# Optimization experiments

Measured on AMD Instinct MI355X. Metric: run time of the kernel, lower is better.

Reference implementation:

```python
import jax, jax.numpy as jnp
import numpy as np

B, T, I = 32, 512, 96
H, M, R, K = 256, 6, 16, 16
TASK, SENS = 32, 64
MPG = M // 3  # mechanisms per group
OUT = 64


def setup_inputs() -> dict:
    key = jax.random.key(0)
    ks = jax.random.split(key, 12)
    inp = {
        'x': jax.random.normal(ks[0], (B, T, I), jnp.float32),
        # stacked per-mechanism LowRankRNNCell params
        'W_ip': jax.random.normal(ks[1], (M, H, H), jnp.float32) / np.sqrt(H),
        'b_ip': jnp.zeros((M, H), jnp.float32),
        'U': jax.random.normal(ks[2], (M, H, R), jnp.float32) / np.sqrt(R),
        'Vr': jax.random.normal(ks[3], (M, R, H), jnp.float32) / np.sqrt(H),
        'cell_bias': jnp.zeros((M, H), jnp.float32),
        'W_in_task': 0.01 * jax.random.normal(ks[4], (MPG, TASK, H), jnp.float32),
        'W_in_sensory': 0.01 * jax.random.normal(ks[5], (MPG, SENS, H), jnp.float32),
        'W_Q': 0.01 * jax.random.normal(ks[6], (M, H, K), jnp.float32),
        'W_K': 0.01 * jax.random.normal(ks[7], (M, H, K), jnp.float32),
        'W_V': 0.01 * jax.random.normal(ks[8], (M, H, H), jnp.float32),
        'W_out': jax.random.normal(ks[9], (H * MPG, OUT), jnp.float32) / np.sqrt(H * MPG),
        'b_out': jnp.zeros((OUT,), jnp.float32),
    }
    return inp


def _rim_forward(x, W_ip, b_ip, U, Vr, cell_bias, W_in_task, W_in_sensory,
                 W_Q, W_K, W_V, W_out, b_out):
    scale = jnp.float32(1.0 / np.sqrt(K))

    def step(Hs, x_t):
        # input routing: group 0 <- task input, group 1 <- sensory, group 2 <- zeros
        x_task = x_t[:, -TASK:]
        x_sens = x_t[:, :-TASK]
        g0 = jnp.einsum('bi,mih->bmh', x_task, W_in_task)
        g1 = jnp.einsum('bi,mih->bmh', x_sens, W_in_sensory)
        A_in = jnp.concatenate([g0, g1, jnp.zeros_like(g0)], axis=1)  # [B,M,H]
        # batched LowRankRNNCell update per mechanism
        inp_part = jnp.einsum('bmi,mih->bmh', A_in, W_ip) + b_ip
        rec = jnp.einsum('bmr,mrh->bmh', jnp.einsum('bmh,mhr->bmr', Hs, U), Vr)
        H_in = jnp.tanh(inp_part + rec + cell_bias)  # [B,M,H]
        # communication attention (exact einsum structure of the original)
        Qc = jnp.einsum('bmh,mhk->bmk', H_in, W_Q)
        Kc = jnp.einsum('bmh,mhk->bmk', H_in, W_K)
        Vc = jnp.einsum('bmh,mhj->bjm', H_in, W_V)  # V_comm[b,h,m]
        attn = jax.nn.softmax(jnp.einsum('bmk,bnk->bmn', Qc, Kc) * scale, axis=-1)
        A_comm = jnp.einsum('bmn,bhm->bnh', attn, Vc)
        H_new = H_in + A_comm
        out = H_new[:, -MPG:].reshape(H_new.shape[0], -1) @ W_out + b_out
        return H_new, (out, H_new, A_in, A_comm, attn)

    H0 = jnp.zeros((x.shape[0], M, H), x.dtype)
    _, (outs, Hseq, Ain_seq, Acomm_seq, attn_seq) = jax.lax.scan(
        step, H0, jnp.swapaxes(x, 0, 1))
    # time-major -> batch-major where the torch code stacks on dim=1 (outputs)
    outputs = jnp.swapaxes(outs, 0, 1)  # [B,T,OUT]
    return outputs, Hseq, Ain_seq, Acomm_seq, attn_seq


def reference(x, W_ip, b_ip, U, Vr, cell_bias, W_in_task, W_in_sensory,
              W_Q, W_K, W_V, W_out, b_out):
    return _rim_forward(x, W_ip, b_ip, U, Vr, cell_bias, W_in_task,
                        W_in_sensory, W_Q, W_K, W_V, W_out, b_out)
```

## Files before the change

### kernel.cpp

```cpp
#include <hip/hip_runtime.h>
#include <math.h>

#define BB 32
#define TT 512
#define II 96
#define HH 256
#define MM 6
#define OUTD 64

#define O_HSEQ  1048576
#define O_AIN   26214400
#define O_ACM   51380224
#define O_ATTN  76546048

#define WS_WEFF 0
#define WS_UT   49152
#define WS_WQT  73728
#define WS_WKT  98304
#define WS_VCH  122880
#define WS_QK   319488
#define WS_FLAG 331776
#define WS_COOP_FLOATS 332288

#define LBAR() asm volatile("s_waitcnt lgkmcnt(0)\n\ts_barrier" ::: "memory")

__global__ __launch_bounds__(256) void rim_weff(
    const float* __restrict__ Wtask, const float* __restrict__ Wsens,
    const float* __restrict__ Wip,
    const float* __restrict__ U, const float* __restrict__ WQ, const float* __restrict__ WK,
    float* __restrict__ Weff, float* __restrict__ Ut, float* __restrict__ WQt, float* __restrict__ WKt)
{
  __shared__ float row[256];
  const int bidx = blockIdx.x;
  const int tid = threadIdx.x;
  if (bidx < 192) {
    int m, i;
    if (bidx < 32)       { m = 0; i = bidx; }
    else if (bidx < 64)  { m = 1; i = bidx - 32; }
    else if (bidx < 128) { m = 2; i = bidx - 64; }
    else                 { m = 3; i = bidx - 128; }
    row[tid] = (m < 2) ? Wtask[(m * 32 + i) * 256 + tid]
                       : Wsens[((m - 2) * 64 + i) * 256 + tid];
    __syncthreads();
    float acc = 0.f;
    const float* wip = Wip + m * 65536 + tid;
    #pragma unroll 8
    for (int j = 0; j < 256; ++j) acc += row[j] * wip[j * 256];
    const int base = (m == 0) ? 0 : (m == 1) ? 8192 : (m == 2) ? 16384 : 32768;
    Weff[base + i * 256 + tid] = acc;
  } else {
    const int p = bidx - 192;
    const int m = p >> 4, r = p & 15;
    Ut [(m * 16 + r) * 256 + tid] = U [m * 4096 + tid * 16 + r];
    WQt[(m * 16 + r) * 256 + tid] = WQ[m * 4096 + tid * 16 + r];
    WKt[(m * 16 + r) * 256 + tid] = WK[m * 4096 + tid * 16 + r];
  }
}

__global__ __launch_bounds__(256) void rim_pre(
    const float* __restrict__ x,
    const float* __restrict__ Wtask, const float* __restrict__ Wsens,
    float* __restrict__ Ain)
{
  __shared__ float xr[16][96];
  const int tid = threadIdx.x;
  const int rb0 = blockIdx.x * 16;
  for (int idx = tid; idx < 16 * 96; idx += 256) {
    int r = idx / 96, c = idx % 96;
    int rb = rb0 + r; int t = rb >> 5, b = rb & 31;
    xr[r][c] = x[(b * TT + t) * II + c];
  }
  __syncthreads();
  const int h = tid;
  float acc[16];

  for (int m = 0; m < 4; ++m) {
    const int cnt  = (m < 2) ? 32 : 64;
    const int xoff = (m < 2) ? 64 : 0;
    const float* W = (m < 2) ? (Wtask + m * 32 * 256) : (Wsens + (m - 2) * 64 * 256);
    #pragma unroll
    for (int r = 0; r < 16; ++r) acc[r] = 0.f;
    for (int i = 0; i < cnt; ++i) {
      float w = W[i * 256 + h];
      #pragma unroll
      for (int r = 0; r < 16; ++r) acc[r] += xr[r][xoff + i] * w;
    }
    #pragma unroll
    for (int r = 0; r < 16; ++r) {
      int rb = rb0 + r; int t = rb >> 5, b = rb & 31;
      Ain[((t * 32 + b) * 6 + m) * 256 + h] = acc[r];
    }
  }
  #pragma unroll
  for (int r = 0; r < 16; ++r) {
    int rb = rb0 + r; int t = rb >> 5, b = rb & 31;
    Ain[((t * 32 + b) * 6 + 4) * 256 + h] = 0.f;
    Ain[((t * 32 + b) * 6 + 5) * 256 + h] = 0.f;
  }
}

__global__ __launch_bounds__(512, 2) void rim_step(
    const float* __restrict__ x,
    const float* __restrict__ Vr, const float* __restrict__ WV,
    const float* __restrict__ bip, const float* __restrict__ cbias,
    const float* __restrict__ UtW, const float* __restrict__ WQtW,
    const float* __restrict__ WKtW, const float* __restrict__ WeffW,
    float* __restrict__ VcHG, float* __restrict__ QKG,
    unsigned int* __restrict__ seqG,
    float* __restrict__ Hseq, float* __restrict__ Acm, float* __restrict__ attnO)
{
  __shared__ __align__(16) float Hl[256];
  __shared__ __align__(16) float Hin[256];
  __shared__ float biasl[256];
  __shared__ float Utl[16][257];
  __shared__ float Vrl[16][257];
  __shared__ float WQtl[16][257];
  __shared__ float WKtl[16][257];
  __shared__ float Weffl[64][256];
  __shared__ float inpl[2][256];
  __shared__ float xl[2][96];
  __shared__ float Vcp1[256];
  __shared__ float tmpUr[16];
  __shared__ float attnl[40];
  __shared__ float qkl[192];

  const int bid = blockIdx.x;
  const int m = bid >> 5;
  const int b = bid & 31;
  const int tid = threadIdx.x;
  const int g32 = tid >> 5, l32 = tid & 31;
  const int h_out = tid & 255, p = tid >> 8;
  const int g16 = tid >> 4, l16 = tid & 15;
  const int w64 = tid >> 6, lane = tid & 63;

  const int base = (m == 0) ? 0 : (m == 1) ? 8192 : (m == 2) ? 16384 : 32768;
  const int cnt  = (m < 2) ? 32 : 64;
  const int xoff = (m < 2) ? 64 : 0;

  for (int i = tid; i < 4096; i += 512) {
    int r = i >> 8, c = i & 255;
    Utl [r][c] = UtW [m * 4096 + i];
    Vrl [r][c] = Vr  [m * 4096 + i];
    WQtl[r][c] = WQtW[m * 4096 + i];
    WKtl[r][c] = WKtW[m * 4096 + i];
  }
  if (m < 4)
    for (int i = tid; i < cnt * 256; i += 512)
      ((float*)Weffl)[i] = WeffW[base + i];
  if (tid < 256) {
    biasl[tid] = bip[m * 256 + tid] + cbias[m * 256 + tid];
    Hl[tid] = 0.f;
  }
  float xreg = 0.f;
  if (m < 4 && tid < 96) {
    xl[0][tid] = x[((size_t)b * TT + 0) * II + tid];
    xreg       = x[((size_t)b * TT + 1) * II + tid];
  }
  float w[128];
  #pragma unroll
  for (int j = 0; j < 128; ++j)
    w[j] = WV[((size_t)(m * 256 + p * 128 + j)) * 256 + h_out];
  __syncthreads();
  if (m < 4 && tid < 256) {
    float a = 0.f;
    for (int i = 0; i < cnt; ++i) a += xl[0][xoff + i] * Weffl[i][tid];
    inpl[0][tid] = a;
  }
  __syncthreads();

  for (int t = 0; t < TT; ++t) {
    const int buf = t & 1;
    const int mb12 = (buf * 32 + b) * 12;
    const int qb   = (buf * 32 + b) * 192;

    if (m < 4 && tid < 96) {
      xl[(t + 1) & 1][tid] = xreg;
      xreg = (t + 2 < TT) ? x[((size_t)b * TT + t + 2) * II + tid] : 0.f;
    }

    {
      float s = 0.f;
      const float* up = &Utl[g32][0];
      #pragma unroll
      for (int h = l32; h < 256; h += 32) s += Hl[h] * up[h];
      #pragma unroll
      for (int off = 16; off > 0; off >>= 1) s += __shfl_down(s, off, 32);
      if (l32 == 0) tmpUr[g32] = s;
    }
    LBAR();

    if (tid < 256) {
      float rec = 0.f;
      #pragma unroll
      for (int r = 0; r < 16; ++r) rec += tmpUr[r] * Vrl[r][tid];
      float inp = (m < 4) ? inpl[buf][tid] : 0.f;
      Hin[tid] = tanhf(inp + rec + biasl[tid]);
    }
    LBAR();

    float accVc = 0.f;
    {
      const float4* h4 = (const float4*)&Hin[p * 128];
      #pragma unroll
      for (int q = 0; q < 32; ++q) {
        float4 hv = h4[q];
        accVc += hv.x * w[4 * q] + hv.y * w[4 * q + 1]
               + hv.z * w[4 * q + 2] + hv.w * w[4 * q + 3];
      }
      __hip_atomic_store(&VcHG[(mb12 + m * 2 + p) * 256 + h_out], accVc,
                         __ATOMIC_RELAXED, __HIP_MEMORY_SCOPE_SYSTEM);
      if (p == 1) Vcp1[h_out] = accVc;
    }
    {
      const int r = g16 & 15;
      const float* wp = (g16 < 16) ? &WQtl[r][0] : &WKtl[r][0];
      float s = 0.f;
      #pragma unroll
      for (int j = 0; j < 16; ++j) { int h = l16 + 16 * j; s += Hin[h] * wp[h]; }
      s += __shfl_down(s, 8, 16);
      s += __shfl_down(s, 4, 16);
      s += __shfl_down(s, 2, 16);
      s += __shfl_down(s, 1, 16);
      if (l16 == 0)
        __hip_atomic_store(&QKG[qb + ((g16 < 16) ? 0 : 96) + m * 16 + r], s,
                           __ATOMIC_RELAXED, __HIP_MEMORY_SCOPE_SYSTEM);
    }
    asm volatile("s_waitcnt vmcnt(0)" ::: "memory");
    LBAR();
    if (tid == 0)
      __hip_atomic_store(&seqG[b * 16 + m], (unsigned)(t + 1),
                         __ATOMIC_RELAXED, __HIP_MEMORY_SCOPE_SYSTEM);

    if (tid >= 256 && m < 4) {
      const int h = tid - 256, nb = (t + 1) & 1;
      float a = 0.f;
      for (int i = 0; i < cnt; ++i) a += xl[nb][xoff + i] * Weffl[i][h];
      inpl[nb][h] = a;
    }
    if (w64 == 0 && lane < 6) {
      while (__hip_atomic_load(&seqG[b * 16 + lane],
                               __ATOMIC_RELAXED, __HIP_MEMORY_SCOPE_SYSTEM)
             < (unsigned)(t + 1)) {}
    }
    LBAR();

    float qv = 0.f;
    if (tid < 192)
      qv = __hip_atomic_load(&QKG[qb + tid],
                             __ATOMIC_RELAXED, __HIP_MEMORY_SCOPE_SYSTEM);
    float vA[6], vB[6];
    if (tid < 256) {
      #pragma unroll
      for (int mm = 0; mm < 6; ++mm) {
        if (mm != m) {
          vA[mm] = __hip_atomic_load(&VcHG[(mb12 + mm * 2 + 0) * 256 + tid],
                                     __ATOMIC_RELAXED, __HIP_MEMORY_SCOPE_SYSTEM);
          vB[mm] = __hip_atomic_load(&VcHG[(mb12 + mm * 2 + 1) * 256 + tid],
                                     __ATOMIC_RELAXED, __HIP_MEMORY_SCOPE_SYSTEM);
        }
      }
    }
    if (tid < 192) qkl[tid] = qv;
    LBAR();

    if (w64 == 0 && lane < 6) {
      float sc[6]; float mx = -1e30f;
      #pragma unroll
      for (int n = 0; n < 6; ++n) {
        float s = 0.f;
        #pragma unroll
        for (int k = 0; k < 16; ++k) s += qkl[lane * 16 + k] * qkl[96 + n * 16 + k];
        sc[n] = s * 0.25f; mx = fmaxf(mx, sc[n]);
      }
      float sm = 0.f;
      #pragma unroll
      for (int n = 0; n < 6; ++n) { sc[n] = expf(sc[n] - mx); sm += sc[n]; }
      float inv = 1.f / sm;
      #pragma unroll
      for (int n = 0; n < 6; ++n) {
        float a = sc[n] * inv;
        attnl[lane * 6 + n] = a;
        if (m == 0) attnO[((size_t)t * 32 + b) * 36 + lane * 6 + n] = a;
      }
    }
    LBAR();

    if (tid < 256) {
      vA[m] = accVc;
      vB[m] = Vcp1[tid];
      float ac = 0.f;
      #pragma unroll
      for (int mm = 0; mm < 6; ++mm) ac += attnl[mm * 6 + m] * (vA[mm] + vB[mm]);
      float hn = Hin[tid] + ac;
      Hl[tid] = hn;
      size_t gi = (((size_t)t * 32 + b) * 6 + m) * 256 + tid;
      Hseq[gi] = hn;
      Acm[gi]  = ac;
    }
    LBAR();
  }
}

__global__ __launch_bounds__(256) void rim_out(
    const float* __restrict__ Hseq, const float* __restrict__ Wout,
    const float* __restrict__ bout, float* __restrict__ out0)
{
  __shared__ float hrow[4][512];
  const int tid = threadIdx.x;
  const int row0 = blockIdx.x * 4;
  for (int i = tid; i < 4 * 512; i += 256) {
    int r = i >> 9, j = i & 511;
    int rb = row0 + r; int b = rb >> 9, t = rb & 511;
    hrow[r][j] = Hseq[((size_t)(t * 32 + b) * 6 + 4 + (j >> 8)) * 256 + (j & 255)];
  }
  __syncthreads();
  const int r = tid >> 6, o = tid & 63;
  const int rb = row0 + r;
  float s = bout[o];
  const float* hp = hrow[r];
  const float* wp = Wout + o;
  #pragma unroll 8
  for (int j = 0; j < 512; ++j) s += hp[j] * wp[(size_t)j * 64];
  out0[(size_t)rb * 64 + o] = s;
}

__global__ __launch_bounds__(512) void rim_loop(
    const float* __restrict__ x,
    const float* __restrict__ Vr, const float* __restrict__ WV,
    const float* __restrict__ Wout, const float* __restrict__ bout,
    const float* __restrict__ bip, const float* __restrict__ cbias,
    const float* __restrict__ Ut, const float* __restrict__ WQt, const float* __restrict__ WKt,
    const float* __restrict__ Weff,
    float* __restrict__ out0, float* __restrict__ Hseq,
    float* __restrict__ Acm, float* __restrict__ attnO)
{
  __shared__ float Hl[6][256];
  __shared__ float Hin[6][256];
  __shared__ float biasl[6][256];
  __shared__ float Vcp[2][6][256];
  __shared__ float tmpUr[6][16];
  __shared__ float Qc[6][16], Kc[6][16];
  __shared__ float attnl[36];
  __shared__ float pout[8][64];
  __shared__ float xl[96];
  __shared__ float inpl[4][256];

  const int b = blockIdx.x;
  const int tid = threadIdx.x;
  const int wid = tid >> 5, lane = tid & 31;

  for (int i = tid; i < 1536; i += 512) {
    int m = i >> 8, h = i & 255;
    biasl[m][h] = bip[i] + cbias[i];
    Hl[m][h] = 0.f;
  }
  __syncthreads();

  for (int t = 0; t < TT; ++t) {
    if (tid < 96) xl[tid] = x[(b * TT + t) * II + tid];
    __syncthreads();
    for (int mh = tid; mh < 1024; mh += 512) {
      int m = mh >> 8, h = mh & 255;
      const int base = (m == 0) ? 0 : (m == 1) ? 8192 : (m == 2) ? 16384 : 32768;
      const int cnt  = (m < 2) ? 32 : 64;
      const int xoff = (m < 2) ? 64 : 0;
      float a = 0.f;
      for (int i = 0; i < cnt; ++i) a += xl[xoff + i] * Weff[base + i * 256 + h];
      inpl[m][h] = a;
    }

    for (int pq = wid; pq < 96; pq += 16) {
      int m = pq >> 4, r = pq & 15;
      const float* up = Ut + (m * 16 + r) * 256;
      float s = 0.f;
      #pragma unroll
      for (int h = lane; h < 256; h += 32) s += Hl[m][h] * up[h];
      #pragma unroll
      for (int off = 16; off > 0; off >>= 1) s += __shfl_down(s, off, 32);
      if (lane == 0) tmpUr[m][r] = s;
    }
    __syncthreads();

    for (int mh = tid; mh < 1536; mh += 512) {
      int m = mh >> 8, h = mh & 255;
      float rec = 0.f;
      const float* vp = Vr + m * 4096 + h;
      #pragma unroll
      for (int r = 0; r < 16; ++r) rec += tmpUr[m][r] * vp[r * 256];
      float pre = (m < 4) ? inpl[m][h] : 0.f;
      Hin[m][h] = tanhf(pre + rec + biasl[m][h]);
    }
    __syncthreads();

    for (int pq = wid; pq < 192; pq += 16) {
      int q = pq % 96;
      int m = q >> 4, k = q & 15;
      const float* wp = ((pq < 96) ? WQt : WKt) + (m * 16 + k) * 256;
      float s = 0.f;
      #pragma unroll
      for (int h = lane; h < 256; h += 32) s += Hin[m][h] * wp[h];
      #pragma unroll
      for (int off = 16; off > 0; off >>= 1) s += __shfl_down(s, off, 32);
      if (lane == 0) { if (pq < 96) Qc[m][k] = s; else Kc[m][k] = s; }
    }

    {
      const int h_out = tid & 255, half = tid >> 8;
      for (int m = 0; m < 6; ++m) {
        const float* wv = WV + ((size_t)(m * 256 + half * 128)) * 256 + h_out;
        const float* hv = &Hin[m][half * 128];
        float s = 0.f;
        #pragma unroll 8
        for (int j = 0; j < 128; ++j) s += hv[j] * wv[(size_t)j * 256];
        Vcp[half][m][h_out] = s;
      }
    }
    __syncthreads();

    if (tid < 36) {
      int m = tid / 6, n = tid % 6;
      float s = 0.f;
      #pragma unroll
      for (int k = 0; k < 16; ++k) s += Qc[m][k] * Kc[n][k];
      attnl[tid] = s * 0.25f;
    }
    __syncthreads();
    if (tid < 6) {
      int m = tid;
      float mx = -1e30f;
      #pragma unroll
      for (int n = 0; n < 6; ++n) mx = fmaxf(mx, attnl[m * 6 + n]);
      float e[6], sm = 0.f;
      #pragma unroll
      for (int n = 0; n < 6; ++n) { e[n] = expf(attnl[m * 6 + n] - mx); sm += e[n]; }
      float inv = 1.f / sm;
      #pragma unroll
      for (int n = 0; n < 6; ++n) attnl[m * 6 + n] = e[n] * inv;
    }
    __syncthreads();
    if (tid < 36) attnO[(size_t)(t * 32 + b) * 36 + tid] = attnl[tid];

    for (int mh = tid; mh < 1536; mh += 512) {
      int n = mh >> 8, h = mh & 255;
      float ac = 0.f;
      #pragma unroll
      for (int m = 0; m < 6; ++m)
        ac += attnl[m * 6 + n] * (Vcp[0][m][h] + Vcp[1][m][h]);
      float hn = Hin[n][h] + ac;
      Hl[n][h] = hn;
      size_t gi = ((size_t)(t * 32 + b) * 6 + n) * 256 + h;
      Hseq[gi] = hn;
      Acm[gi]  = ac;
    }
    __syncthreads();

    {
      const int o = tid & 63, js = tid >> 6;
      const float* hp = &Hl[4][0];
      const float* wp = Wout + (size_t)(js * 64) * 64 + o;
      float s = 0.f;
      #pragma unroll 8
      for (int jj = 0; jj < 64; ++jj) s += hp[js * 64 + jj] * wp[(size_t)jj * 64];
      pout[js][o] = s;
    }
    __syncthreads();
    if (tid < 64) {
      float s = bout[tid];
      #pragma unroll
      for (int js = 0; js < 8; ++js) s += pout[js][tid];
      out0[(size_t)(b * TT + t) * 64 + tid] = s;
    }
  }
}

extern "C" void kernel_launch(void* const* d_in, const int* in_sizes, int n_in,
                              void* d_out, int out_size, void* d_ws, size_t ws_size,
                              hipStream_t stream) {
  const float* x    = (const float*)d_in[0];
  const float* W_ip = (const float*)d_in[1];
  const float* b_ip = (const float*)d_in[2];
  const float* U    = (const float*)d_in[3];
  const float* Vr   = (const float*)d_in[4];
  const float* cb   = (const float*)d_in[5];
  const float* Wt   = (const float*)d_in[6];
  const float* Wsn  = (const float*)d_in[7];
  const float* WQ   = (const float*)d_in[8];
  const float* WK   = (const float*)d_in[9];
  const float* WV   = (const float*)d_in[10];
  const float* Wo   = (const float*)d_in[11];
  const float* bo   = (const float*)d_in[12];

  float* out  = (float*)d_out;
  float* Hseq = out + O_HSEQ;
  float* Ain  = out + O_AIN;
  float* Acm  = out + O_ACM;
  float* attn = out + O_ATTN;

  float* ws   = (float*)d_ws;
  float* Weff = ws + WS_WEFF;
  float* Ut   = ws + WS_UT;
  float* WQt  = ws + WS_WQT;
  float* WKt  = ws + WS_WKT;

  hipLaunchKernelGGL(rim_weff, dim3(288), dim3(256), 0, stream,
                     Wt, Wsn, W_ip, U, WQ, WK, Weff, Ut, WQt, WKt);
  hipLaunchKernelGGL(rim_pre, dim3(1024), dim3(256), 0, stream,
                     x, Wt, Wsn, Ain);

  if (ws_size >= (size_t)WS_COOP_FLOATS * sizeof(float)) {
    float* VcHG = ws + WS_VCH;
    float* QKG  = ws + WS_QK;
    unsigned int* seqG = (unsigned int*)(ws + WS_FLAG);
    hipMemsetAsync((void*)seqG, 0, 512 * sizeof(unsigned int), stream);

    void* args[] = { (void*)&x, (void*)&Vr, (void*)&WV, (void*)&b_ip, (void*)&cb,
                     (void*)&Ut, (void*)&WQt, (void*)&WKt, (void*)&Weff,
                     (void*)&VcHG, (void*)&QKG, (void*)&seqG,
                     (void*)&Hseq, (void*)&Acm, (void*)&attn };
    hipLaunchCooperativeKernel((void*)rim_step, dim3(192), dim3(512), args, 0, stream);

    hipLaunchKernelGGL(rim_out, dim3(4096), dim3(256), 0, stream,
                       Hseq, Wo, bo, out);
  } else {
    hipLaunchKernelGGL(rim_loop, dim3(32), dim3(512), 0, stream,
                       x, Vr, WV, Wo, bo, b_ip, cb, Ut, WQt, WKt, Weff,
                       out, Hseq, Acm, attn);
  }
}
```

Measured before the change: 2.577 ms.

## Replace block barriers with per-wave flags and wave-local attention softmax

Each wavefront now publishes its own progress flag after its Q/K and V_comm stores drain, instead of a block barrier followed by a single per-block flag. Consumer waves spin on all 48 per-wave flags. Each of the four consumer waves then recomputes the 6x6 attention softmax with cross-lane shuffles in place of LDS staging. This removes several block-wide barriers per timestep from the serial recurrence. In exchange, every consumer wave polls 48 flags and does the attention and V loads redundantly, and the flag array and workspace grow.

After: 3.162 ms. 22.7% more time.

```diff
diff --git a/kernel.cpp b/kernel.cpp
--- a/kernel.cpp
+++ b/kernel.cpp
@@ -20,7 +20,7 @@
 #define WS_VCH  122880
 #define WS_QK   319488
 #define WS_FLAG 331776
-#define WS_COOP_FLOATS 332288
+#define WS_COOP_FLOATS 333824
 
 #define LBAR() asm volatile("s_waitcnt lgkmcnt(0)\n\ts_barrier" ::: "memory")
 
@@ -119,10 +119,8 @@
   __shared__ float Weffl[64][256];
   __shared__ float inpl[2][256];
   __shared__ float xl[2][96];
-  __shared__ float Vcp1[256];
   __shared__ float tmpUr[16];
-  __shared__ float attnl[40];
-  __shared__ float qkl[192];
+  __shared__ float qklw[4][192];
 
   const int bid = blockIdx.x;
   const int m = bid >> 5;
@@ -172,6 +170,7 @@
     const int buf = t & 1;
     const int mb12 = (buf * 32 + b) * 12;
     const int qb   = (buf * 32 + b) * 192;
+    const unsigned target = (unsigned)(t + 1);
 
     if (m < 4 && tid < 96) {
       xl[(t + 1) & 1][tid] = xreg;
@@ -198,19 +197,6 @@
     }
     LBAR();
 
-    float accVc = 0.f;
-    {
-      const float4* h4 = (const float4*)&Hin[p * 128];
-      #pragma unroll
-      for (int q = 0; q < 32; ++q) {
-        float4 hv = h4[q];
-        accVc += hv.x * w[4 * q] + hv.y * w[4 * q + 1]
-               + hv.z * w[4 * q + 2] + hv.w * w[4 * q + 3];
-      }
-      __hip_atomic_store(&VcHG[(mb12 + m * 2 + p) * 256 + h_out], accVc,
-                         __ATOMIC_RELAXED, __HIP_MEMORY_SCOPE_SYSTEM);
-      if (p == 1) Vcp1[h_out] = accVc;
-    }
     {
       const int r = g16 & 15;
       const float* wp = (g16 < 16) ? &WQtl[r][0] : &WKtl[r][0];
@@ -225,77 +211,91 @@
         __hip_atomic_store(&QKG[qb + ((g16 < 16) ? 0 : 96) + m * 16 + r], s,
                            __ATOMIC_RELAXED, __HIP_MEMORY_SCOPE_SYSTEM);
     }
+    float accVc = 0.f;
+    {
+      const float4* h4 = (const float4*)&Hin[p * 128];
+      #pragma unroll
+      for (int q = 0; q < 32; ++q) {
+        float4 hv = h4[q];
+        accVc += hv.x * w[4 * q] + hv.y * w[4 * q + 1]
+               + hv.z * w[4 * q + 2] + hv.w * w[4 * q + 3];
+      }
+      __hip_atomic_store(&VcHG[(mb12 + m * 2 + p) * 256 + h_out], accVc,
+                         __ATOMIC_RELAXED, __HIP_MEMORY_SCOPE_SYSTEM);
+    }
     asm volatile("s_waitcnt vmcnt(0)" ::: "memory");
-    LBAR();
-    if (tid == 0)
-      __hip_atomic_store(&seqG[b * 16 + m], (unsigned)(t + 1),
+    if (lane == 0)
+      __hip_atomic_store(&seqG[b * 64 + m * 8 + w64], target,
                          __ATOMIC_RELAXED, __HIP_MEMORY_SCOPE_SYSTEM);
 
-    if (tid >= 256 && m < 4) {
-      const int h = tid - 256, nb = (t + 1) & 1;
+    if (w64 < 4) {
+      if (lane < 48) {
+        while (__hip_atomic_load(&seqG[b * 64 + lane],
+                                 __ATOMIC_RELAXED, __HIP_MEMORY_SCOPE_SYSTEM)
+               < target) { }
+      }
+      float q0 = __hip_atomic_load(&QKG[qb + lane],       __ATOMIC_RELAXED, __HIP_MEMORY_SCOPE_SYSTEM);
+      float q1 = __hip_atomic_load(&QKG[qb + 64 + lane],  __ATOMIC_RELAXED, __HIP_MEMORY_SCOPE_SYSTEM);
+      float q2 = __hip_atomic_load(&QKG[qb + 128 + lane], __ATOMIC_RELAXED, __HIP_MEMORY_SCOPE_SYSTEM);
+      float vA[6], vB[6];
+      #pragma unroll
+      for (int mm = 0; mm < 6; ++mm) {
+        if (mm != m)
+          vA[mm] = __hip_atomic_load(&VcHG[(mb12 + mm * 2 + 0) * 256 + h_out],
+                                     __ATOMIC_RELAXED, __HIP_MEMORY_SCOPE_SYSTEM);
+        vB[mm] = __hip_atomic_load(&VcHG[(mb12 + mm * 2 + 1) * 256 + h_out],
+                                   __ATOMIC_RELAXED, __HIP_MEMORY_SCOPE_SYSTEM);
+      }
+      vA[m] = accVc;
+
+      qklw[w64][lane]       = q0;
+      qklw[w64][64 + lane]  = q1;
+      qklw[w64][128 + lane] = q2;
+
       float a = 0.f;
-      for (int i = 0; i < cnt; ++i) a += xl[nb][xoff + i] * Weffl[i][h];
-      inpl[nb][h] = a;
-    }
-    if (w64 == 0 && lane < 6) {
-      while (__hip_atomic_load(&seqG[b * 16 + lane],
-                               __ATOMIC_RELAXED, __HIP_MEMORY_SCOPE_SYSTEM)
-             < (unsigned)(t + 1)) {}
-    }
-    LBAR();
-
-    float qv = 0.f;
-    if (tid < 192)
-      qv = __hip_atomic_load(&QKG[qb + tid],
-                             __ATOMIC_RELAXED, __HIP_MEMORY_SCOPE_SYSTEM);
-    float vA[6], vB[6];
-    if (tid < 256) {
+      {
+        const int mm6 = (lane < 36) ? (lane / 6) : 0;
+        const int nn  = (lane < 36) ? (lane % 6) : 0;
+        if (lane < 36) {
+          const float* qw = &qklw[w64][mm6 * 16];
+          const float* kw = &qklw[w64][96 + nn * 16];
+          float s = 0.f;
+          #pragma unroll
+          for (int k = 0; k < 16; ++k) s += qw[k] * kw[k];
+          s *= 0.25f;
+          float mx = s;
+          #pragma unroll
+          for (int d = 1; d < 6; ++d)
+            mx = fmaxf(mx, __shfl(s, mm6 * 6 + ((nn + d) % 6), 64));
+          float e = __expf(s - mx);
+          float sm = e;
+          #pragma unroll
+          for (int d = 1; d < 6; ++d)
+            sm += __shfl(e, mm6 * 6 + ((nn + d) % 6), 64);
+          a = e / sm;
+        }
+      }
+      if (m == 0 && w64 == 0 && lane < 36)
+        attnO[((size_t)t * 32 + b) * 36 + lane] = a;
+
+      float ac = 0.f;
       #pragma unroll
       for (int mm = 0; mm < 6; ++mm) {
-        if (mm != m) {
-          vA[mm] = __hip_atomic_load(&VcHG[(mb12 + mm * 2 + 0) * 256 + tid],
-                                     __ATOMIC_RELAXED, __HIP_MEMORY_SCOPE_SYSTEM);
-          vB[mm] = __hip_atomic_load(&VcHG[(mb12 + mm * 2 + 1) * 256 + tid],
-                                     __ATOMIC_RELAXED, __HIP_MEMORY_SCOPE_SYSTEM);
-        }
-      }
-    }
-    if (tid < 192) qkl[tid] = qv;
-    LBAR();
-
-    if (w64 == 0 && lane < 6) {
-      float sc[6]; float mx = -1e30f;
-      #pragma unroll
-      for (int n = 0; n < 6; ++n) {
-        float s = 0.f;
-        #pragma unroll
-        for (int k = 0; k < 16; ++k) s += qkl[lane * 16 + k] * qkl[96 + n * 16 + k];
-        sc[n] = s * 0.25f; mx = fmaxf(mx, sc[n]);
-      }
-      float sm = 0.f;
-      #pragma unroll
-      for (int n = 0; n < 6; ++n) { sc[n] = expf(sc[n] - mx); sm += sc[n]; }
-      float inv = 1.f / sm;
-      #pragma unroll
-      for (int n = 0; n < 6; ++n) {
-        float a = sc[n] * inv;
-        attnl[lane * 6 + n] = a;
-        if (m == 0) attnO[((size_t)t * 32 + b) * 36 + lane * 6 + n] = a;
-      }
-    }
-    LBAR();
-
-    if (tid < 256) {
-      vA[m] = accVc;
-      vB[m] = Vcp1[tid];
-      float ac = 0.f;
-      #pragma unroll
-      for (int mm = 0; mm < 6; ++mm) ac += attnl[mm * 6 + m] * (vA[mm] + vB[mm]);
+        float amm = __shfl(a, mm * 6 + m, 64);
+        ac += amm * (vA[mm] + vB[mm]);
+      }
       float hn = Hin[tid] + ac;
       Hl[tid] = hn;
       size_t gi = (((size_t)t * 32 + b) * 6 + m) * 256 + tid;
       Hseq[gi] = hn;
       Acm[gi]  = ac;
+    } else {
+      if (m < 4) {
+        const int h = tid - 256, nb = (t + 1) & 1;
+        float a = 0.f;
+        for (int i = 0; i < cnt; ++i) a += xl[nb][xoff + i] * Weffl[i][h];
+        inpl[nb][h] = a;
+      }
     }
     LBAR();
   }
@@ -511,7 +511,7 @@
     float* VcHG = ws + WS_VCH;
     float* QKG  = ws + WS_QK;
     unsigned int* seqG = (unsigned int*)(ws + WS_FLAG);
-    hipMemsetAsync((void*)seqG, 0, 512 * sizeof(unsigned int), stream);
+    hipMemsetAsync((void*)seqG, 0, 2048 * sizeof(unsigned int), stream);
 
     void* args[] = { (void*)&x, (void*)&Vr, (void*)&WV, (void*)&b_ip, (void*)&cb,
                      (void*)&Ut, (void*)&WQt, (void*)&WKt, (void*)&Weff,
```

## Probe L2 coherence at startup and use cheaper L2-scoped cross-block exchange

Applied to the files above, without the earlier changes.

Remaps block IDs so that the six mechanism blocks of a batch element sit on the same XCD (bid&7 pattern). A startup handshake checks whether plain stores and sc0 loads are visible between those blocks through L2. If so, it switches the per-step flag and data exchange from system-scope atomics to volatile stores and L2 loads. It also pre-sums the two V halves locally so each block publishes one vector instead of two, halving exchange traffic, and issues the loads in batches. The cost is reliance on a hardware XCD-placement assumption, guarded by a runtime probe with fallback, plus extra startup spin handshakes.

After: 2.797 ms. 1.09x slower.

```diff
diff --git a/kernel.cpp b/kernel.cpp
--- a/kernel.cpp
+++ b/kernel.cpp
@@ -4,9 +4,6 @@
 #define BB 32
 #define TT 512
 #define II 96
-#define HH 256
-#define MM 6
-#define OUTD 64
 
 #define O_HSEQ  1048576
 #define O_AIN   26214400
@@ -17,12 +14,71 @@
 #define WS_UT   49152
 #define WS_WQT  73728
 #define WS_WKT  98304
-#define WS_VCH  122880
-#define WS_QK   319488
-#define WS_FLAG 331776
-#define WS_COOP_FLOATS 332288
+#define WS_VC   122880
+#define WS_QK   221184
+#define WS_FLAG 233472
+#define WS_PRBF 233984
+#define WS_PRBD 234176
+#define WS_BMP  234368
+#define WS_NONCE 235328
+#define WS_COOP_FLOATS 235360
 
 #define LBAR() asm volatile("s_waitcnt lgkmcnt(0)\n\ts_barrier" ::: "memory")
+
+__device__ __forceinline__ float sysldf(const float* p) {
+  return __hip_atomic_load(p, __ATOMIC_RELAXED, __HIP_MEMORY_SCOPE_SYSTEM);
+}
+__device__ __forceinline__ void sysstf(float* p, float v) {
+  __hip_atomic_store(p, v, __ATOMIC_RELAXED, __HIP_MEMORY_SCOPE_SYSTEM);
+}
+__device__ __forceinline__ unsigned sysld32(const unsigned* p) {
+  return __hip_atomic_load(p, __ATOMIC_RELAXED, __HIP_MEMORY_SCOPE_SYSTEM);
+}
+__device__ __forceinline__ void sysst32(unsigned* p, unsigned v) {
+  __hip_atomic_store(p, v, __ATOMIC_RELAXED, __HIP_MEMORY_SCOPE_SYSTEM);
+}
+
+__device__ __forceinline__ unsigned ldl2u(const unsigned* p) {
+  unsigned v;
+  asm volatile("global_load_dword %0, %1, off sc0\n\ts_waitcnt vmcnt(0)"
+               : "=&v"(v) : "v"(p) : "memory");
+  return v;
+}
+__device__ __forceinline__ void ldl2x6(
+    float& d0, float& d1, float& d2, float& d3, float& d4, float& d5,
+    const float* p0, const float* p1, const float* p2,
+    const float* p3, const float* p4, const float* p5) {
+  asm volatile(
+    "global_load_dword %0, %6, off sc0\n\t"
+    "global_load_dword %1, %7, off sc0\n\t"
+    "global_load_dword %2, %8, off sc0\n\t"
+    "global_load_dword %3, %9, off sc0\n\t"
+    "global_load_dword %4, %10, off sc0\n\t"
+    "global_load_dword %5, %11, off sc0\n\t"
+    "s_waitcnt vmcnt(0)"
+    : "=&v"(d0), "=&v"(d1), "=&v"(d2), "=&v"(d3), "=&v"(d4), "=&v"(d5)
+    : "v"(p0), "v"(p1), "v"(p2), "v"(p3), "v"(p4), "v"(p5)
+    : "memory");
+  __builtin_amdgcn_sched_barrier(0);
+}
+__device__ __forceinline__ void ldl2x7(
+    float& d0, float& d1, float& d2, float& d3, float& d4, float& d5, float& d6,
+    const float* p0, const float* p1, const float* p2, const float* p3,
+    const float* p4, const float* p5, const float* p6) {
+  asm volatile(
+    "global_load_dword %0, %7, off sc0\n\t"
+    "global_load_dword %1, %8, off sc0\n\t"
+    "global_load_dword %2, %9, off sc0\n\t"
+    "global_load_dword %3, %10, off sc0\n\t"
+    "global_load_dword %4, %11, off sc0\n\t"
+    "global_load_dword %5, %12, off sc0\n\t"
+    "global_load_dword %6, %13, off sc0\n\t"
+    "s_waitcnt vmcnt(0)"
+    : "=&v"(d0), "=&v"(d1), "=&v"(d2), "=&v"(d3), "=&v"(d4), "=&v"(d5), "=&v"(d6)
+    : "v"(p0), "v"(p1), "v"(p2), "v"(p3), "v"(p4), "v"(p5), "v"(p6)
+    : "memory");
+  __builtin_amdgcn_sched_barrier(0);
+}
 
 __global__ __launch_bounds__(256) void rim_weff(
     const float* __restrict__ Wtask, const float* __restrict__ Wsens,
@@ -105,8 +161,10 @@
     const float* __restrict__ bip, const float* __restrict__ cbias,
     const float* __restrict__ UtW, const float* __restrict__ WQtW,
     const float* __restrict__ WKtW, const float* __restrict__ WeffW,
-    float* __restrict__ VcHG, float* __restrict__ QKG,
-    unsigned int* __restrict__ seqG,
+    float* __restrict__ VcG, float* __restrict__ QKG,
+    unsigned* __restrict__ seqG,
+    unsigned* __restrict__ prbF, unsigned* __restrict__ prbD,
+    unsigned* __restrict__ bmpG, unsigned* __restrict__ nonceG,
     float* __restrict__ Hseq, float* __restrict__ Acm, float* __restrict__ attnO)
 {
   __shared__ __align__(16) float Hl[256];
@@ -123,10 +181,12 @@
   __shared__ float tmpUr[16];
   __shared__ float attnl[40];
   __shared__ float qkl[192];
+  __shared__ int fastS;
 
   const int bid = blockIdx.x;
-  const int m = bid >> 5;
-  const int b = bid & 31;
+  const int rrm = bid & 7, qq = bid >> 3;
+  const int m = qq % 6;
+  const int b = rrm + 8 * (qq / 6);
   const int tid = threadIdx.x;
   const int g32 = tid >> 5, l32 = tid & 31;
   const int h_out = tid & 255, p = tid >> 8;
@@ -160,7 +220,90 @@
   #pragma unroll
   for (int j = 0; j < 128; ++j)
     w[j] = WV[((size_t)(m * 256 + p * 128 + j)) * 256 + h_out];
+
+  if (tid == 0) {
+    unsigned nonce;
+    if (m == 0) {
+      unsigned long long tt = clock64();
+      nonce = (unsigned)(tt ^ (tt >> 17) ^ 0x5bd1e995u) & 0x7FFFFFFFu;
+      if (nonce == 0) nonce = 1;
+      sysst32(&nonceG[b], 0x80000000u | nonce);
+    } else {
+      unsigned e;
+      do { e = sysld32(&nonceG[b]); } while (!(e & 0x80000000u));
+      nonce = e & 0x7FFFFFFFu;
+    }
+    const unsigned pbase = nonce * 2654435761u;
+    bool ok = true;
+
+    {
+      unsigned myp = (pbase + (unsigned)bid * 193u + 0x11110000u) | 1u;
+      *(volatile unsigned*)&prbF[bid] = myp;
+      asm volatile("s_waitcnt vmcnt(0)" ::: "memory");
+      unsigned seen = 0;
+      for (int it = 0; it < 3000 && seen != 0x3Fu; ++it) {
+        int mm = it % 6;
+        if (!(seen & (1u << mm))) {
+          int pbm = (b & 7) + 8 * (mm + 6 * (b >> 3));
+          unsigned want = (pbase + (unsigned)pbm * 193u + 0x11110000u) | 1u;
+          if (ldl2u(&prbF[pbm]) == want) seen |= (1u << mm);
+        }
+      }
+      sysst32(&bmpG[0 * 192 + bid], 0x40000000u | seen);
+      for (int mm = 0; mm < 6; ++mm) {
+        int pbm = (b & 7) + 8 * (mm + 6 * (b >> 3));
+        unsigned e;
+        do { e = sysld32(&bmpG[0 * 192 + pbm]); } while (!(e & 0x40000000u));
+        ok = ok && ((e & 0x3Fu) == 0x3Fu);
+      }
+    }
+
+    for (int r = 1; r <= 3; ++r) {
+      if (ok) {
+        unsigned dp = (pbase + (unsigned)bid * 97u + (unsigned)r * 0x010F0000u) | 1u;
+        unsigned fp = (pbase + (unsigned)bid * 57u + (unsigned)r * 0x00F10000u + 0x20000000u) | 1u;
+        *(volatile unsigned*)&prbD[bid] = dp;
+        asm volatile("s_waitcnt vmcnt(0)" ::: "memory");
+        *(volatile unsigned*)&prbF[bid] = fp;
+        asm volatile("s_waitcnt vmcnt(0)" ::: "memory");
+        unsigned good = 0, fail = 0;
+        for (int it = 0; it < 1500 && good != 0x3Fu && !fail; ++it) {
+          int mm = it % 6;
+          if (!(good & (1u << mm))) {
+            int pbm = (b & 7) + 8 * (mm + 6 * (b >> 3));
+            unsigned fexp = (pbase + (unsigned)pbm * 57u + (unsigned)r * 0x00F10000u + 0x20000000u) | 1u;
+            if (ldl2u(&prbF[pbm]) == fexp) {
+              unsigned dexp = (pbase + (unsigned)pbm * 97u + (unsigned)r * 0x010F0000u) | 1u;
+              if (ldl2u(&prbD[pbm]) == dexp) good |= (1u << mm);
+              else fail = 1;
+            }
+          }
+        }
+        sysst32(&bmpG[r * 192 + bid], 0x40000000u | good | (fail ? 0x80u : 0u));
+        for (int mm = 0; mm < 6; ++mm) {
+          int pbm = (b & 7) + 8 * (mm + 6 * (b >> 3));
+          unsigned e;
+          do { e = sysld32(&bmpG[r * 192 + pbm]); } while (!(e & 0x40000000u));
+          ok = ok && ((e & 0xBFu) == 0x3Fu);
+        }
+      }
+    }
+
+    if (ok) {
+      *(volatile unsigned*)&seqG[b * 16 + m] = 0u;
+      asm volatile("s_waitcnt vmcnt(0)" ::: "memory");
+      sysst32(&bmpG[4 * 192 + bid], 0x40000000u);
+      for (int mm = 0; mm < 6; ++mm) {
+        int pbm = (b & 7) + 8 * (mm + 6 * (b >> 3));
+        unsigned e;
+        do { e = sysld32(&bmpG[4 * 192 + pbm]); } while (!(e & 0x40000000u));
+      }
+    }
+    fastS = ok ? 1 : 0;
+  }
   __syncthreads();
+  const bool fast = (fastS != 0);
+
   if (m < 4 && tid < 256) {
     float a = 0.f;
     for (int i = 0; i < cnt; ++i) a += xl[0][xoff + i] * Weffl[i][tid];
@@ -170,8 +313,9 @@
 
   for (int t = 0; t < TT; ++t) {
     const int buf = t & 1;
-    const int mb12 = (buf * 32 + b) * 12;
-    const int qb   = (buf * 32 + b) * 192;
+    const unsigned target = (unsigned)(t + 1);
+    const int vb6 = (buf * 32 + b) * 6;
+    const int qb  = (buf * 32 + b) * 192;
 
     if (m < 4 && tid < 96) {
       xl[(t + 1) & 1][tid] = xreg;
@@ -198,19 +342,6 @@
     }
     LBAR();
 
-    float accVc = 0.f;
-    {
-      const float4* h4 = (const float4*)&Hin[p * 128];
-      #pragma unroll
-      for (int q = 0; q < 32; ++q) {
-        float4 hv = h4[q];
-        accVc += hv.x * w[4 * q] + hv.y * w[4 * q + 1]
-               + hv.z * w[4 * q + 2] + hv.w * w[4 * q + 3];
-      }
-      __hip_atomic_store(&VcHG[(mb12 + m * 2 + p) * 256 + h_out], accVc,
-                         __ATOMIC_RELAXED, __HIP_MEMORY_SCOPE_SYSTEM);
-      if (p == 1) Vcp1[h_out] = accVc;
-    }
     {
       const int r = g16 & 15;
       const float* wp = (g16 < 16) ? &WQtl[r][0] : &WKtl[r][0];
@@ -221,15 +352,39 @@
       s += __shfl_down(s, 4, 16);
       s += __shfl_down(s, 2, 16);
       s += __shfl_down(s, 1, 16);
-      if (l16 == 0)
-        __hip_atomic_store(&QKG[qb + ((g16 < 16) ? 0 : 96) + m * 16 + r], s,
-                           __ATOMIC_RELAXED, __HIP_MEMORY_SCOPE_SYSTEM);
+      if (l16 == 0) {
+        float* pq = &QKG[qb + ((g16 < 16) ? 0 : 96) + m * 16 + r];
+        if (fast) *(volatile float*)pq = s;
+        else      sysstf(pq, s);
+      }
+    }
+    float accVc = 0.f;
+    {
+      const float4* h4 = (const float4*)&Hin[p * 128];
+      #pragma unroll
+      for (int q = 0; q < 32; ++q) {
+        float4 hv = h4[q];
+        accVc += hv.x * w[4 * q] + hv.y * w[4 * q + 1]
+               + hv.z * w[4 * q + 2] + hv.w * w[4 * q + 3];
+      }
+    }
+    if (p == 1) Vcp1[h_out] = accVc;
+    LBAR();
+
+    float vown = 0.f;
+    if (tid < 256) {
+      vown = accVc + Vcp1[tid];
+      float* pp = &VcG[(vb6 + m) * 256 + tid];
+      if (fast) *(volatile float*)pp = vown;
+      else      sysstf(pp, vown);
     }
     asm volatile("s_waitcnt vmcnt(0)" ::: "memory");
     LBAR();
-    if (tid == 0)
-      __hip_atomic_store(&seqG[b * 16 + m], (unsigned)(t + 1),
-                         __ATOMIC_RELAXED, __HIP_MEMORY_SCOPE_SYSTEM);
+    if (tid == 0) {
+      unsigned* ps = &seqG[b * 16 + m];
+      if (fast) *(volatile unsigned*)ps = target;
+      else      sysst32(ps, target);
+    }
 
     if (tid >= 256 && m < 4) {
       const int h = tid - 256, nb = (t + 1) & 1;
@@ -238,28 +393,39 @@
       inpl[nb][h] = a;
     }
     if (w64 == 0 && lane < 6) {
-      while (__hip_atomic_load(&seqG[b * 16 + lane],
-                               __ATOMIC_RELAXED, __HIP_MEMORY_SCOPE_SYSTEM)
-             < (unsigned)(t + 1)) {}
-    }
-    LBAR();
-
-    float qv = 0.f;
-    if (tid < 192)
-      qv = __hip_atomic_load(&QKG[qb + tid],
-                             __ATOMIC_RELAXED, __HIP_MEMORY_SCOPE_SYSTEM);
-    float vA[6], vB[6];
-    if (tid < 256) {
-      #pragma unroll
-      for (int mm = 0; mm < 6; ++mm) {
-        if (mm != m) {
-          vA[mm] = __hip_atomic_load(&VcHG[(mb12 + mm * 2 + 0) * 256 + tid],
-                                     __ATOMIC_RELAXED, __HIP_MEMORY_SCOPE_SYSTEM);
-          vB[mm] = __hip_atomic_load(&VcHG[(mb12 + mm * 2 + 1) * 256 + tid],
-                                     __ATOMIC_RELAXED, __HIP_MEMORY_SCOPE_SYSTEM);
-        }
-      }
-    }
+      const unsigned* ps = &seqG[b * 16 + lane];
+      if (fast) { while (ldl2u(ps)   < target) { } }
+      else      { while (sysld32(ps) < target) { } }
+    }
+    LBAR();
+
+    float vC[6]; float qv = 0.f;
+    if (tid < 192) {
+      if (fast) {
+        ldl2x7(qv, vC[0], vC[1], vC[2], vC[3], vC[4], vC[5],
+               &QKG[qb + tid],
+               &VcG[(vb6 + 0) * 256 + tid], &VcG[(vb6 + 1) * 256 + tid],
+               &VcG[(vb6 + 2) * 256 + tid], &VcG[(vb6 + 3) * 256 + tid],
+               &VcG[(vb6 + 4) * 256 + tid], &VcG[(vb6 + 5) * 256 + tid]);
+      } else {
+        qv = sysldf(&QKG[qb + tid]);
+        #pragma unroll
+        for (int mm = 0; mm < 6; ++mm)
+          vC[mm] = sysldf(&VcG[(vb6 + mm) * 256 + tid]);
+      }
+    } else if (tid < 256) {
+      if (fast) {
+        ldl2x6(vC[0], vC[1], vC[2], vC[3], vC[4], vC[5],
+               &VcG[(vb6 + 0) * 256 + tid], &VcG[(vb6 + 1) * 256 + tid],
+               &VcG[(vb6 + 2) * 256 + tid], &VcG[(vb6 + 3) * 256 + tid],
+               &VcG[(vb6 + 4) * 256 + tid], &VcG[(vb6 + 5) * 256 + tid]);
+      } else {
+        #pragma unroll
+        for (int mm = 0; mm < 6; ++mm)
+          vC[mm] = sysldf(&VcG[(vb6 + mm) * 256 + tid]);
+      }
+    }
+    if (tid < 256) vC[m] = vown;
     if (tid < 192) qkl[tid] = qv;
     LBAR();
 
@@ -286,11 +452,9 @@
     LBAR();
 
     if (tid < 256) {
-      vA[m] = accVc;
-      vB[m] = Vcp1[tid];
       float ac = 0.f;
       #pragma unroll
-      for (int mm = 0; mm < 6; ++mm) ac += attnl[mm * 6 + m] * (vA[mm] + vB[mm]);
+      for (int mm = 0; mm < 6; ++mm) ac += attnl[mm * 6 + m] * vC[mm];
       float hn = Hin[tid] + ac;
       Hl[tid] = hn;
       size_t gi = (((size_t)t * 32 + b) * 6 + m) * 256 + tid;
@@ -508,14 +672,20 @@
                      x, Wt, Wsn, Ain);
 
   if (ws_size >= (size_t)WS_COOP_FLOATS * sizeof(float)) {
-    float* VcHG = ws + WS_VCH;
-    float* QKG  = ws + WS_QK;
-    unsigned int* seqG = (unsigned int*)(ws + WS_FLAG);
-    hipMemsetAsync((void*)seqG, 0, 512 * sizeof(unsigned int), stream);
+    float* VcG = ws + WS_VC;
+    float* QKG = ws + WS_QK;
+    unsigned* seqG   = (unsigned*)(ws + WS_FLAG);
+    unsigned* prbF   = (unsigned*)(ws + WS_PRBF);
+    unsigned* prbD   = (unsigned*)(ws + WS_PRBD);
+    unsigned* bmpG   = (unsigned*)(ws + WS_BMP);
+    unsigned* nonceG = (unsigned*)(ws + WS_NONCE);
+    hipMemsetAsync((void*)seqG, 0,
+                   (size_t)(WS_COOP_FLOATS - WS_FLAG) * sizeof(float), stream);
 
     void* args[] = { (void*)&x, (void*)&Vr, (void*)&WV, (void*)&b_ip, (void*)&cb,
                      (void*)&Ut, (void*)&WQt, (void*)&WKt, (void*)&Weff,
-                     (void*)&VcHG, (void*)&QKG, (void*)&seqG,
+                     (void*)&VcG, (void*)&QKG, (void*)&seqG,
+                     (void*)&prbF, (void*)&prbD, (void*)&bmpG, (void*)&nonceG,
                      (void*)&Hseq, (void*)&Acm, (void*)&attn };
     hipLaunchCooperativeKernel((void*)rim_step, dim3(192), dim3(512), args, 0, stream);
 
```
